# Performance work log

Hardware: AMD Instinct MI355X
Metric: run time of the kernel (lower is better)

## Reference

```python
import jax, jax.numpy as jnp
import numpy as np

N_NODES = 50000
N_EDGES = 800000
DIM_IN = 128
DIM_OUT = 64


def setup_inputs() -> dict:
    key = jax.random.key(0)
    k1, k2, k3, k4 = jax.random.split(key, 4)
    x = jax.random.normal(k1, (N_NODES, DIM_IN), dtype=jnp.float32)
    edge_index = jax.random.randint(k2, (2, N_EDGES), 0, N_NODES, dtype=jnp.int64)
    W = jax.random.normal(k3, (DIM_IN, DIM_OUT), dtype=jnp.float32) / np.sqrt(DIM_IN)
    b = jax.random.normal(k4, (DIM_OUT,), dtype=jnp.float32) * 0.01
    return {"x": x, "edge_index": edge_index, "W": W, "b": b}


def reference(x, edge_index, W, b):
    # Faithful PyG GCNConv: add self-loops, symmetric deg normalization,
    # linear transform then normalized scatter-add aggregation, then bias.
    N = x.shape[0]
    h = x @ W  # [N, dim_out] — transform before propagate (PyG order)

    loops = jnp.arange(N, dtype=edge_index.dtype)
    src = jnp.concatenate([edge_index[0], loops])  # [E+N]
    dst = jnp.concatenate([edge_index[1], loops])  # [E+N]

    ones = jnp.ones(src.shape[0], dtype=h.dtype)
    deg = jax.ops.segment_sum(ones, dst, num_segments=N)  # in-degree incl. self-loop
    dinv = jnp.where(deg > 0, jax.lax.rsqrt(deg), 0.0)
    norm = dinv[src] * dinv[dst]  # [E+N]

    msgs = h[src] * norm[:, None]  # gather + scale
    out = jax.ops.segment_sum(msgs, dst, num_segments=N) + b  # scatter-add
    return jax.nn.log_softmax(out, axis=1)
```

## Files before the change

kernel.cpp:

```cpp
#include <hip/hip_runtime.h>
#include <hip/hip_fp16.h>
#include <cstdint>
#include <cstddef>

#define N_NODES 50000
#define N_EDGES 800000
#define DIM_IN  128
#define DIM_OUT 64

#define BSHIFT  6
#define BNODES  64
#define NB      1024
#define NBK     ((N_NODES + BNODES - 1) / BNODES)
#define EB      4096
#define SORTB   ((N_EDGES + EB - 1) / EB)
#define NE4     (N_EDGES / 4)
#define CAPB    1280
#define GROWS   128
#define GEMMB   ((N_NODES + GROWS - 1) / GROWS)
#define NEGRP   ((N_NODES + 31) / 32)

typedef _Float16 f16x8 __attribute__((ext_vector_type(8)));
typedef _Float16 f16x4 __attribute__((ext_vector_type(4)));
typedef float    f32x4 __attribute__((ext_vector_type(4)));

__global__ __launch_bounds__(256) void k_zero(int* __restrict__ gcnt) {
    const int i = blockIdx.x * 256 + threadIdx.x;
    if (i < NB) gcnt[i] = 0;
}

__global__ __launch_bounds__(256) void kFG(const int* __restrict__ ei,
                                           int* __restrict__ gcnt,
                                           unsigned* __restrict__ pairs,
                                           const float* __restrict__ x,
                                           const float* __restrict__ W,
                                           __half* __restrict__ h) {
    const int t = threadIdx.x;
    if (blockIdx.x < SORTB) {
        __shared__ int hcnt[NB];
        __shared__ int cur[NB];
        const int blk = blockIdx.x;
        for (int i = t; i < NB; i += 256) hcnt[i] = 0;
        __syncthreads();
        const int4* src4 = (const int4*)ei;
        const int4* dst4 = (const int4*)(ei + N_EDGES);
        const int g0 = blk * (EB / 4);
#pragma unroll
        for (int it = 0; it < EB / 1024; ++it) {
            const int g = g0 + it * 256 + t;
            if (g < NE4) {
                const int4 d = dst4[g];
                atomicAdd(&hcnt[d.x >> BSHIFT], 1);
                atomicAdd(&hcnt[d.y >> BSHIFT], 1);
                atomicAdd(&hcnt[d.z >> BSHIFT], 1);
                atomicAdd(&hcnt[d.w >> BSHIFT], 1);
            }
        }
        __syncthreads();
        for (int i = t; i < NB; i += 256) {
            const int c = hcnt[i];
            const int base = c ? atomicAdd(&gcnt[i], c) : 0;
            cur[i] = i * CAPB + base;
        }
        __syncthreads();
#pragma unroll
        for (int it = 0; it < EB / 1024; ++it) {
            const int g = g0 + it * 256 + t;
            if (g < NE4) {
                const int4 sv = src4[g];
                const int4 dv = dst4[g];
                int b, p;
                b = dv.x >> BSHIFT; p = atomicAdd(&cur[b], 1);
                if (p < b * CAPB + CAPB) pairs[p] = ((unsigned)sv.x << 16) | (unsigned)dv.x;
                b = dv.y >> BSHIFT; p = atomicAdd(&cur[b], 1);
                if (p < b * CAPB + CAPB) pairs[p] = ((unsigned)sv.y << 16) | (unsigned)dv.y;
                b = dv.z >> BSHIFT; p = atomicAdd(&cur[b], 1);
                if (p < b * CAPB + CAPB) pairs[p] = ((unsigned)sv.z << 16) | (unsigned)dv.z;
                b = dv.w >> BSHIFT; p = atomicAdd(&cur[b], 1);
                if (p < b * CAPB + CAPB) pairs[p] = ((unsigned)sv.w << 16) | (unsigned)dv.w;
            }
        }
    } else {
        const int u = blockIdx.x - SORTB;
        const int w = t >> 6;
        const int l = t & 63;
        const int q = l >> 4;
        const int m16 = l & 15;

        f16x8 bf[4][4];
#pragma unroll
        for (int kc = 0; kc < 4; ++kc)
#pragma unroll
            for (int ct = 0; ct < 4; ++ct) {
                const float* wp = W + (size_t)(kc * 32 + q * 8) * DIM_OUT + ct * 16 + m16;
                f16x8 v;
#pragma unroll
                for (int j = 0; j < 8; ++j) v[j] = (_Float16)wp[(size_t)j * DIM_OUT];
                bf[kc][ct] = v;
            }

        const int base = u * GROWS + w * 32;
#pragma unroll
        for (int rt = 0; rt < 2; ++rt) {
            const int m0 = base + rt * 16;
            int mrow = m0 + m16;
            if (mrow >= N_NODES) mrow = N_NODES - 1;

            f16x8 af[4];
#pragma unroll
            for (int kc = 0; kc < 4; ++kc) {
                const float4* xp = (const float4*)(x + (size_t)mrow * DIM_IN + kc * 32 + q * 8);
                const float4 p0 = xp[0], p1 = xp[1];
                f16x8 a;
                a[0] = (_Float16)p0.x; a[1] = (_Float16)p0.y;
                a[2] = (_Float16)p0.z; a[3] = (_Float16)p0.w;
                a[4] = (_Float16)p1.x; a[5] = (_Float16)p1.y;
                a[6] = (_Float16)p1.z; a[7] = (_Float16)p1.w;
                af[kc] = a;
            }

            f32x4 acc[4];
#pragma unroll
            for (int ct = 0; ct < 4; ++ct) acc[ct] = (f32x4){0.f, 0.f, 0.f, 0.f};
#pragma unroll
            for (int kc = 0; kc < 4; ++kc)
#pragma unroll
                for (int ct = 0; ct < 4; ++ct)
                    acc[ct] = __builtin_amdgcn_mfma_f32_16x16x32_f16(af[kc], bf[kc][ct], acc[ct], 0, 0, 0);

#pragma unroll
            for (int reg = 0; reg < 4; ++reg) {
                const int r = m0 + q * 4 + reg;
                if (r < N_NODES) {
#pragma unroll
                    for (int ct = 0; ct < 4; ++ct)
                        h[(size_t)r * DIM_OUT + ct * 16 + m16] = __float2half(acc[ct][reg]);
                }
            }
        }
    }
}

__global__ __launch_bounds__(256) void kSort(const unsigned* __restrict__ pairs,
                                             const int* __restrict__ gcnt,
                                             unsigned short* __restrict__ csr,
                                             int2* __restrict__ nodeoff2,
                                             __half* __restrict__ h) {
    __shared__ int cnt[BNODES];
    __shared__ int cur[BNODES];
    __shared__ float sdinv[BNODES];
    const int b = blockIdx.x, t = threadIdx.x;
    const int eb = b * CAPB;
    const int count = min(gcnt[b], CAPB);
    const int ee = eb + count;

    if (t < BNODES) cnt[t] = 0;
    __syncthreads();

    {
        int i = eb + t;
        for (; i + 768 < ee; i += 1024) {
            const unsigned p0 = pairs[i];
            const unsigned p1 = pairs[i + 256];
            const unsigned p2 = pairs[i + 512];
            const unsigned p3 = pairs[i + 768];
            atomicAdd(&cnt[p0 & (BNODES - 1)], 1);
            atomicAdd(&cnt[p1 & (BNODES - 1)], 1);
            atomicAdd(&cnt[p2 & (BNODES - 1)], 1);
            atomicAdd(&cnt[p3 & (BNODES - 1)], 1);
        }
        for (; i < ee; i += 256) atomicAdd(&cnt[pairs[i] & (BNODES - 1)], 1);
    }
    __syncthreads();

    if (t < 64) {
        const int lane = t;
        const int v = cnt[lane];
        int xs = v;
#pragma unroll
        for (int off = 1; off < 64; off <<= 1) {
            int y = __shfl_up(xs, off);
            if (lane >= off) xs += y;
        }
        const int excl = xs - v;
        cur[lane] = eb + excl;
        sdinv[lane] = rsqrtf((float)(v + 1));
        const int n = (b << BSHIFT) + lane;
        if (n < N_NODES) nodeoff2[n] = make_int2(eb + excl, v);
    }
    __syncthreads();

    {
        f16x8* h8w = (f16x8*)h;
        for (int idx = t; idx < BNODES * 8; idx += 256) {
            const int r = idx >> 3;
            const int n = (b << BSHIFT) + r;
            if (n < N_NODES) {
                const float d = sdinv[r];
                f16x8 v = h8w[n * 8 + (idx & 7)];
#pragma unroll
                for (int j = 0; j < 8; ++j) v[j] = (_Float16)((float)v[j] * d);
                h8w[n * 8 + (idx & 7)] = v;
            }
        }
    }

    {
        int i = eb + t;
        for (; i + 768 < ee; i += 1024) {
            const unsigned p0 = pairs[i];
            const unsigned p1 = pairs[i + 256];
            const unsigned p2 = pairs[i + 512];
            const unsigned p3 = pairs[i + 768];
            int q;
            q = atomicAdd(&cur[p0 & (BNODES - 1)], 1); csr[q] = (unsigned short)(p0 >> 16);
            q = atomicAdd(&cur[p1 & (BNODES - 1)], 1); csr[q] = (unsigned short)(p1 >> 16);
            q = atomicAdd(&cur[p2 & (BNODES - 1)], 1); csr[q] = (unsigned short)(p2 >> 16);
            q = atomicAdd(&cur[p3 & (BNODES - 1)], 1); csr[q] = (unsigned short)(p3 >> 16);
        }
        for (; i < ee; i += 256) {
            const unsigned p = pairs[i];
            const int q = atomicAdd(&cur[p & (BNODES - 1)], 1);
            csr[q] = (unsigned short)(p >> 16);
        }
    }
}

__global__ __launch_bounds__(256) void kE_agg(const int2* __restrict__ nodeoff2,
                                              const unsigned short* __restrict__ csr,
                                              const __half* __restrict__ h,
                                              const float* __restrict__ bvec,
                                              float* __restrict__ out) {
    const int t = threadIdx.x;
    const int ew = t >> 3, sl = t & 7;
    const int n = blockIdx.x * 32 + ew;
    if (n >= N_NODES) return;
    const f16x8* __restrict__ h8 = (const f16x8*)h;

    const int2 off = nodeoff2[n];
    const int s0 = off.x, s1 = off.x + off.y;

    const f16x8 hv = h8[n * 8 + sl];
    float a[8];
#pragma unroll
    for (int j = 0; j < 8; ++j) a[j] = (float)hv[j];

    int i = s0;
    for (; i + 4 <= s1; i += 4) {
        const int c0 = csr[i + 0];
        const int c1 = csr[i + 1];
        const int c2 = csr[i + 2];
        const int c3 = csr[i + 3];
        const f16x8 v0 = h8[c0 * 8 + sl];
        const f16x8 v1 = h8[c1 * 8 + sl];
        const f16x8 v2 = h8[c2 * 8 + sl];
        const f16x8 v3 = h8[c3 * 8 + sl];
#pragma unroll
        for (int j = 0; j < 8; ++j)
            a[j] += (float)v0[j] + (float)v1[j] + (float)v2[j] + (float)v3[j];
    }
    for (; i < s1; ++i) {
        const f16x8 v0 = h8[csr[i] * 8 + sl];
#pragma unroll
        for (int j = 0; j < 8; ++j) a[j] += (float)v0[j];
    }

    const float4 b0 = *(const float4*)&bvec[8 * sl];
    const float4 b1 = *(const float4*)&bvec[8 * sl + 4];
    const float di = rsqrtf((float)(off.y + 1));
    float v[8];
    v[0] = a[0] * di + b0.x; v[1] = a[1] * di + b0.y;
    v[2] = a[2] * di + b0.z; v[3] = a[3] * di + b0.w;
    v[4] = a[4] * di + b1.x; v[5] = a[5] * di + b1.y;
    v[6] = a[6] * di + b1.z; v[7] = a[7] * di + b1.w;

    float m = v[0];
#pragma unroll
    for (int j = 1; j < 8; ++j) m = fmaxf(m, v[j]);
#pragma unroll
    for (int o = 4; o > 0; o >>= 1) m = fmaxf(m, __shfl_xor(m, o));
    float s = 0.f;
#pragma unroll
    for (int j = 0; j < 8; ++j) s += __expf(v[j] - m);
#pragma unroll
    for (int o = 4; o > 0; o >>= 1) s += __shfl_xor(s, o);
    const float ls = m + __logf(s);

    float4 o0, o1;
    o0.x = v[0] - ls; o0.y = v[1] - ls; o0.z = v[2] - ls; o0.w = v[3] - ls;
    o1.x = v[4] - ls; o1.y = v[5] - ls; o1.z = v[6] - ls; o1.w = v[7] - ls;
    *(float4*)&out[(size_t)n * DIM_OUT + 8 * sl]     = o0;
    *(float4*)&out[(size_t)n * DIM_OUT + 8 * sl + 4] = o1;
}

extern "C" void kernel_launch(void* const* d_in, const int* in_sizes, int n_in,
                              void* d_out, int out_size, void* d_ws, size_t ws_size,
                              hipStream_t stream) {
    const float* x  = (const float*)d_in[0];
    const int*   ei = (const int*)d_in[1];
    const float* W  = (const float*)d_in[2];
    const float* b  = (const float*)d_in[3];
    float* out = (float*)d_out;

    char* ws = (char*)d_ws;
    __half*         h        = (__half*)ws;         ws += (size_t)N_NODES * DIM_OUT * sizeof(__half);
    unsigned*       pairs    = (unsigned*)ws;       ws += (size_t)NB * CAPB * sizeof(unsigned);
    unsigned short* csr      = (unsigned short*)ws; ws += (size_t)NB * CAPB * sizeof(unsigned short);
    int2*           nodeoff2 = (int2*)ws;           ws += (size_t)N_NODES * sizeof(int2);
    int*            gcnt     = (int*)ws;            ws += (size_t)NB * sizeof(int);

    k_zero<<<(NB + 255) / 256, 256, 0, stream>>>(gcnt);
    kFG   <<<SORTB + GEMMB, 256, 0, stream>>>(ei, gcnt, pairs, x, W, h);
    kSort <<<NBK, 256, 0, stream>>>(pairs, gcnt, csr, nodeoff2, h);
    kE_agg<<<NEGRP, 256, 0, stream>>>(nodeoff2, csr, h, b, out);
}
```

Baseline: 114.8 us.

## Fuse bucket sort with aggregation using shared-memory CSR and global degree array

Merges the per-bucket sort kernel and the aggregation kernel into one 512-thread kernel. The CSR now lives in shared memory, so the global csr and nodeoff arrays and one launch are dropped. Source rows of h are no longer prescaled in place. Instead a global per-node degree array is built with atomics in the first kernel, and each gathered neighbour is scaled by its rsqrt(deg+1) at aggregation time. This removes the csr write and read round trip and the h rescale pass, at the cost of 800k extra global atomics and an extra degree gather per edge.

```diff
diff --git a/kernel.cpp b/kernel.cpp
--- a/kernel.cpp
+++ b/kernel.cpp
@@ -18,20 +18,21 @@
 #define CAPB    1280
 #define GROWS   128
 #define GEMMB   ((N_NODES + GROWS - 1) / GROWS)
-#define NEGRP   ((N_NODES + 31) / 32)
 
 typedef _Float16 f16x8 __attribute__((ext_vector_type(8)));
-typedef _Float16 f16x4 __attribute__((ext_vector_type(4)));
 typedef float    f32x4 __attribute__((ext_vector_type(4)));
 
-__global__ __launch_bounds__(256) void k_zero(int* __restrict__ gcnt) {
+__global__ __launch_bounds__(256) void k_zero(int* __restrict__ gcnt,
+                                              int* __restrict__ deg) {
     const int i = blockIdx.x * 256 + threadIdx.x;
     if (i < NB) gcnt[i] = 0;
+    if (i < N_NODES) deg[i] = 0;
 }
 
 __global__ __launch_bounds__(256) void kFG(const int* __restrict__ ei,
                                            int* __restrict__ gcnt,
                                            unsigned* __restrict__ pairs,
+                                           int* __restrict__ deg,
                                            const float* __restrict__ x,
                                            const float* __restrict__ W,
                                            __half* __restrict__ h) {
@@ -54,6 +55,10 @@
                 atomicAdd(&hcnt[d.y >> BSHIFT], 1);
                 atomicAdd(&hcnt[d.z >> BSHIFT], 1);
                 atomicAdd(&hcnt[d.w >> BSHIFT], 1);
+                atomicAdd(&deg[d.x], 1);
+                atomicAdd(&deg[d.y], 1);
+                atomicAdd(&deg[d.z], 1);
+                atomicAdd(&deg[d.w], 1);
             }
         }
         __syncthreads();
@@ -141,14 +146,16 @@
     }
 }
 
-__global__ __launch_bounds__(256) void kSort(const unsigned* __restrict__ pairs,
-                                             const int* __restrict__ gcnt,
-                                             unsigned short* __restrict__ csr,
-                                             int2* __restrict__ nodeoff2,
-                                             __half* __restrict__ h) {
+__global__ __launch_bounds__(512) void kSortE(const unsigned* __restrict__ pairs,
+                                              const int* __restrict__ gcnt,
+                                              const int* __restrict__ deg,
+                                              const __half* __restrict__ h,
+                                              const float* __restrict__ bvec,
+                                              float* __restrict__ out) {
     __shared__ int cnt[BNODES];
     __shared__ int cur[BNODES];
     __shared__ float sdinv[BNODES];
+    __shared__ unsigned short lcsr[CAPB];
     const int b = blockIdx.x, t = threadIdx.x;
     const int eb = b * CAPB;
     const int count = min(gcnt[b], CAPB);
@@ -157,20 +164,8 @@
     if (t < BNODES) cnt[t] = 0;
     __syncthreads();
 
-    {
-        int i = eb + t;
-        for (; i + 768 < ee; i += 1024) {
-            const unsigned p0 = pairs[i];
-            const unsigned p1 = pairs[i + 256];
-            const unsigned p2 = pairs[i + 512];
-            const unsigned p3 = pairs[i + 768];
-            atomicAdd(&cnt[p0 & (BNODES - 1)], 1);
-            atomicAdd(&cnt[p1 & (BNODES - 1)], 1);
-            atomicAdd(&cnt[p2 & (BNODES - 1)], 1);
-            atomicAdd(&cnt[p3 & (BNODES - 1)], 1);
-        }
-        for (; i < ee; i += 256) atomicAdd(&cnt[pairs[i] & (BNODES - 1)], 1);
-    }
+    for (int i = eb + t; i < ee; i += 512)
+        atomicAdd(&cnt[pairs[i] & (BNODES - 1)], 1);
     __syncthreads();
 
     if (t < 64) {
@@ -182,97 +177,65 @@
             int y = __shfl_up(xs, off);
             if (lane >= off) xs += y;
         }
-        const int excl = xs - v;
-        cur[lane] = eb + excl;
+        cur[lane] = xs - v;
         sdinv[lane] = rsqrtf((float)(v + 1));
-        const int n = (b << BSHIFT) + lane;
-        if (n < N_NODES) nodeoff2[n] = make_int2(eb + excl, v);
-    }
-    __syncthreads();
-
-    {
-        f16x8* h8w = (f16x8*)h;
-        for (int idx = t; idx < BNODES * 8; idx += 256) {
-            const int r = idx >> 3;
-            const int n = (b << BSHIFT) + r;
-            if (n < N_NODES) {
-                const float d = sdinv[r];
-                f16x8 v = h8w[n * 8 + (idx & 7)];
-#pragma unroll
-                for (int j = 0; j < 8; ++j) v[j] = (_Float16)((float)v[j] * d);
-                h8w[n * 8 + (idx & 7)] = v;
-            }
-        }
-    }
-
-    {
-        int i = eb + t;
-        for (; i + 768 < ee; i += 1024) {
-            const unsigned p0 = pairs[i];
-            const unsigned p1 = pairs[i + 256];
-            const unsigned p2 = pairs[i + 512];
-            const unsigned p3 = pairs[i + 768];
-            int q;
-            q = atomicAdd(&cur[p0 & (BNODES - 1)], 1); csr[q] = (unsigned short)(p0 >> 16);
-            q = atomicAdd(&cur[p1 & (BNODES - 1)], 1); csr[q] = (unsigned short)(p1 >> 16);
-            q = atomicAdd(&cur[p2 & (BNODES - 1)], 1); csr[q] = (unsigned short)(p2 >> 16);
-            q = atomicAdd(&cur[p3 & (BNODES - 1)], 1); csr[q] = (unsigned short)(p3 >> 16);
-        }
-        for (; i < ee; i += 256) {
-            const unsigned p = pairs[i];
-            const int q = atomicAdd(&cur[p & (BNODES - 1)], 1);
-            csr[q] = (unsigned short)(p >> 16);
-        }
-    }
-}
-
-__global__ __launch_bounds__(256) void kE_agg(const int2* __restrict__ nodeoff2,
-                                              const unsigned short* __restrict__ csr,
-                                              const __half* __restrict__ h,
-                                              const float* __restrict__ bvec,
-                                              float* __restrict__ out) {
-    const int t = threadIdx.x;
-    const int ew = t >> 3, sl = t & 7;
-    const int n = blockIdx.x * 32 + ew;
+    }
+    __syncthreads();
+
+    for (int i = eb + t; i < ee; i += 512) {
+        const unsigned p = pairs[i];
+        const int q = atomicAdd(&cur[p & (BNODES - 1)], 1);
+        lcsr[q] = (unsigned short)(p >> 16);
+    }
+    __syncthreads();
+
+    const int r = t >> 3, sl = t & 7;
+    const int n = (b << BSHIFT) + r;
     if (n >= N_NODES) return;
     const f16x8* __restrict__ h8 = (const f16x8*)h;
 
-    const int2 off = nodeoff2[n];
-    const int s0 = off.x, s1 = off.x + off.y;
-
-    const f16x8 hv = h8[n * 8 + sl];
+    const int s1 = cur[r];
+    const int s0 = s1 - cnt[r];
+    const float din = sdinv[r];
+
+    const f16x8 hv = h8[(size_t)n * 8 + sl];
     float a[8];
 #pragma unroll
-    for (int j = 0; j < 8; ++j) a[j] = (float)hv[j];
+    for (int j = 0; j < 8; ++j) a[j] = (float)hv[j] * din;
 
     int i = s0;
-    for (; i + 4 <= s1; i += 4) {
-        const int c0 = csr[i + 0];
-        const int c1 = csr[i + 1];
-        const int c2 = csr[i + 2];
-        const int c3 = csr[i + 3];
-        const f16x8 v0 = h8[c0 * 8 + sl];
-        const f16x8 v1 = h8[c1 * 8 + sl];
-        const f16x8 v2 = h8[c2 * 8 + sl];
-        const f16x8 v3 = h8[c3 * 8 + sl];
-#pragma unroll
-        for (int j = 0; j < 8; ++j)
-            a[j] += (float)v0[j] + (float)v1[j] + (float)v2[j] + (float)v3[j];
+    for (; i + 8 <= s1; i += 8) {
+        int   c[8];
+        float dv[8];
+        f16x8 vv[8];
+#pragma unroll
+        for (int j = 0; j < 8; ++j) c[j] = lcsr[i + j];
+#pragma unroll
+        for (int j = 0; j < 8; ++j) dv[j] = (float)deg[c[j]];
+#pragma unroll
+        for (int j = 0; j < 8; ++j) vv[j] = h8[(size_t)c[j] * 8 + sl];
+#pragma unroll
+        for (int j = 0; j < 8; ++j) {
+            const float s = rsqrtf(dv[j] + 1.0f);
+#pragma unroll
+            for (int k = 0; k < 8; ++k) a[k] += (float)vv[j][k] * s;
+        }
     }
     for (; i < s1; ++i) {
-        const f16x8 v0 = h8[csr[i] * 8 + sl];
-#pragma unroll
-        for (int j = 0; j < 8; ++j) a[j] += (float)v0[j];
+        const int c = lcsr[i];
+        const float s = rsqrtf((float)deg[c] + 1.0f);
+        const f16x8 v0 = h8[(size_t)c * 8 + sl];
+#pragma unroll
+        for (int j = 0; j < 8; ++j) a[j] += (float)v0[j] * s;
     }
 
     const float4 b0 = *(const float4*)&bvec[8 * sl];
     const float4 b1 = *(const float4*)&bvec[8 * sl + 4];
-    const float di = rsqrtf((float)(off.y + 1));
     float v[8];
-    v[0] = a[0] * di + b0.x; v[1] = a[1] * di + b0.y;
-    v[2] = a[2] * di + b0.z; v[3] = a[3] * di + b0.w;
-    v[4] = a[4] * di + b1.x; v[5] = a[5] * di + b1.y;
-    v[6] = a[6] * di + b1.z; v[7] = a[7] * di + b1.w;
+    v[0] = a[0] * din + b0.x; v[1] = a[1] * din + b0.y;
+    v[2] = a[2] * din + b0.z; v[3] = a[3] * din + b0.w;
+    v[4] = a[4] * din + b1.x; v[5] = a[5] * din + b1.y;
+    v[6] = a[6] * din + b1.z; v[7] = a[7] * din + b1.w;
 
     float m = v[0];
 #pragma unroll
@@ -303,14 +266,12 @@
     float* out = (float*)d_out;
 
     char* ws = (char*)d_ws;
-    __half*         h        = (__half*)ws;         ws += (size_t)N_NODES * DIM_OUT * sizeof(__half);
-    unsigned*       pairs    = (unsigned*)ws;       ws += (size_t)NB * CAPB * sizeof(unsigned);
-    unsigned short* csr      = (unsigned short*)ws; ws += (size_t)NB * CAPB * sizeof(unsigned short);
-    int2*           nodeoff2 = (int2*)ws;           ws += (size_t)N_NODES * sizeof(int2);
-    int*            gcnt     = (int*)ws;            ws += (size_t)NB * sizeof(int);
-
-    k_zero<<<(NB + 255) / 256, 256, 0, stream>>>(gcnt);
-    kFG   <<<SORTB + GEMMB, 256, 0, stream>>>(ei, gcnt, pairs, x, W, h);
-    kSort <<<NBK, 256, 0, stream>>>(pairs, gcnt, csr, nodeoff2, h);
-    kE_agg<<<NEGRP, 256, 0, stream>>>(nodeoff2, csr, h, b, out);
-}
+    __half*   h     = (__half*)ws;   ws += (size_t)N_NODES * DIM_OUT * sizeof(__half);
+    unsigned* pairs = (unsigned*)ws; ws += (size_t)NB * CAPB * sizeof(unsigned);
+    int*      gcnt  = (int*)ws;      ws += (size_t)NB * sizeof(int);
+    int*      deg   = (int*)ws;      ws += (size_t)N_NODES * sizeof(int);
+
+    k_zero<<<(N_NODES + 255) / 256, 256, 0, stream>>>(gcnt, deg);
+    kFG   <<<SORTB + GEMMB, 256, 0, stream>>>(ei, gcnt, pairs, deg, x, W, h);
+    kSortE<<<NBK, 512, 0, stream>>>(pairs, gcnt, deg, h, b, out);
+}
```

New measurement: 146.0 us. 27.1% more time.

## Shrink edge-bucketing blocks and pad global bucket counters to separate cache lines

Applied to the files above, without the earlier changes.

Each sort block now handles 1024 edges, one int4 per thread, instead of 4096. That gives four times as many blocks and keeps the dst vector in registers across both passes, so it is not reloaded. The global per-bucket counters are padded by 16 ints (64 bytes), so each counter sits on its own cache line and atomics to neighbouring buckets stop contending. In exchange, the number of global atomics per bucket rises roughly fourfold, each block zeroes and scans a 1024-entry shared histogram for fewer edges, and within a bucket the edges are split into more, smaller contiguous runs.

```diff
diff --git a/kernel.cpp b/kernel.cpp
--- a/kernel.cpp
+++ b/kernel.cpp
@@ -12,21 +12,21 @@
 #define BNODES  64
 #define NB      1024
 #define NBK     ((N_NODES + BNODES - 1) / BNODES)
-#define EB      4096
+#define EB      1024
 #define SORTB   ((N_EDGES + EB - 1) / EB)
 #define NE4     (N_EDGES / 4)
 #define CAPB    1280
 #define GROWS   128
 #define GEMMB   ((N_NODES + GROWS - 1) / GROWS)
 #define NEGRP   ((N_NODES + 31) / 32)
+#define GPAD    16
 
 typedef _Float16 f16x8 __attribute__((ext_vector_type(8)));
-typedef _Float16 f16x4 __attribute__((ext_vector_type(4)));
 typedef float    f32x4 __attribute__((ext_vector_type(4)));
 
 __global__ __launch_bounds__(256) void k_zero(int* __restrict__ gcnt) {
     const int i = blockIdx.x * 256 + threadIdx.x;
-    if (i < NB) gcnt[i] = 0;
+    if (i < NB * GPAD) gcnt[i] = 0;
 }
 
 __global__ __launch_bounds__(256) void kFG(const int* __restrict__ ei,
@@ -44,41 +44,34 @@
         __syncthreads();
         const int4* src4 = (const int4*)ei;
         const int4* dst4 = (const int4*)(ei + N_EDGES);
-        const int g0 = blk * (EB / 4);
-#pragma unroll
-        for (int it = 0; it < EB / 1024; ++it) {
-            const int g = g0 + it * 256 + t;
-            if (g < NE4) {
-                const int4 d = dst4[g];
-                atomicAdd(&hcnt[d.x >> BSHIFT], 1);
-                atomicAdd(&hcnt[d.y >> BSHIFT], 1);
-                atomicAdd(&hcnt[d.z >> BSHIFT], 1);
-                atomicAdd(&hcnt[d.w >> BSHIFT], 1);
-            }
+        const int g = blk * (EB / 4) + t;
+        int4 sv, dv;
+        const bool live = (g < NE4);
+        if (live) {
+            dv = dst4[g];
+            atomicAdd(&hcnt[dv.x >> BSHIFT], 1);
+            atomicAdd(&hcnt[dv.y >> BSHIFT], 1);
+            atomicAdd(&hcnt[dv.z >> BSHIFT], 1);
+            atomicAdd(&hcnt[dv.w >> BSHIFT], 1);
         }
         __syncthreads();
         for (int i = t; i < NB; i += 256) {
             const int c = hcnt[i];
-            const int base = c ? atomicAdd(&gcnt[i], c) : 0;
+            const int base = c ? atomicAdd(&gcnt[i * GPAD], c) : 0;
             cur[i] = i * CAPB + base;
         }
         __syncthreads();
-#pragma unroll
-        for (int it = 0; it < EB / 1024; ++it) {
-            const int g = g0 + it * 256 + t;
-            if (g < NE4) {
-                const int4 sv = src4[g];
-                const int4 dv = dst4[g];
-                int b, p;
-                b = dv.x >> BSHIFT; p = atomicAdd(&cur[b], 1);
-                if (p < b * CAPB + CAPB) pairs[p] = ((unsigned)sv.x << 16) | (unsigned)dv.x;
-                b = dv.y >> BSHIFT; p = atomicAdd(&cur[b], 1);
-                if (p < b * CAPB + CAPB) pairs[p] = ((unsigned)sv.y << 16) | (unsigned)dv.y;
-                b = dv.z >> BSHIFT; p = atomicAdd(&cur[b], 1);
-                if (p < b * CAPB + CAPB) pairs[p] = ((unsigned)sv.z << 16) | (unsigned)dv.z;
-                b = dv.w >> BSHIFT; p = atomicAdd(&cur[b], 1);
-                if (p < b * CAPB + CAPB) pairs[p] = ((unsigned)sv.w << 16) | (unsigned)dv.w;
-            }
+        if (live) {
+            sv = src4[g];
+            int b, p;
+            b = dv.x >> BSHIFT; p = atomicAdd(&cur[b], 1);
+            if (p < b * CAPB + CAPB) pairs[p] = ((unsigned)sv.x << 16) | (unsigned)dv.x;
+            b = dv.y >> BSHIFT; p = atomicAdd(&cur[b], 1);
+            if (p < b * CAPB + CAPB) pairs[p] = ((unsigned)sv.y << 16) | (unsigned)dv.y;
+            b = dv.z >> BSHIFT; p = atomicAdd(&cur[b], 1);
+            if (p < b * CAPB + CAPB) pairs[p] = ((unsigned)sv.z << 16) | (unsigned)dv.z;
+            b = dv.w >> BSHIFT; p = atomicAdd(&cur[b], 1);
+            if (p < b * CAPB + CAPB) pairs[p] = ((unsigned)sv.w << 16) | (unsigned)dv.w;
         }
     } else {
         const int u = blockIdx.x - SORTB;
@@ -151,7 +144,7 @@
     __shared__ float sdinv[BNODES];
     const int b = blockIdx.x, t = threadIdx.x;
     const int eb = b * CAPB;
-    const int count = min(gcnt[b], CAPB);
+    const int count = min(gcnt[b * GPAD], CAPB);
     const int ee = eb + count;
 
     if (t < BNODES) cnt[t] = 0;
@@ -307,9 +300,9 @@
     unsigned*       pairs    = (unsigned*)ws;       ws += (size_t)NB * CAPB * sizeof(unsigned);
     unsigned short* csr      = (unsigned short*)ws; ws += (size_t)NB * CAPB * sizeof(unsigned short);
     int2*           nodeoff2 = (int2*)ws;           ws += (size_t)N_NODES * sizeof(int2);
-    int*            gcnt     = (int*)ws;            ws += (size_t)NB * sizeof(int);
-
-    k_zero<<<(NB + 255) / 256, 256, 0, stream>>>(gcnt);
+    int*            gcnt     = (int*)ws;            ws += (size_t)NB * GPAD * sizeof(int);
+
+    k_zero<<<(NB * GPAD + 255) / 256, 256, 0, stream>>>(gcnt);
     kFG   <<<SORTB + GEMMB, 256, 0, stream>>>(ei, gcnt, pairs, x, W, h);
     kSort <<<NBK, 256, 0, stream>>>(pairs, gcnt, csr, nodeoff2, h);
     kE_agg<<<NEGRP, 256, 0, stream>>>(nodeoff2, csr, h, b, out);
```

Result: slower. 149.4 us (+30.2%).
